# Optimization experiments

Hardware: AMD Instinct MI355X
Metric: run time of the kernel (lower is better)

## Reference

```python
import jax, jax.numpy as jnp
import numpy as np

B, S, D, H, DC, HC, M = 2, 2048, 1024, 16, 64, 16, 4096
DH = D // H  # head_dim = 64


def _ln(x, g, b, eps=1e-5):
    m = jnp.mean(x, axis=-1, keepdims=True)
    v = jnp.var(x, axis=-1, keepdims=True)
    return (x - m) * jax.lax.rsqrt(v + eps) * g + b


def setup_inputs() -> dict:
    key = jax.random.key(0)
    ks = jax.random.split(key, 10)
    def w(k, shape, fan_in):
        return jax.random.normal(k, shape, jnp.float32) * (fan_in ** -0.5)
    return {
        "h": jax.random.normal(ks[0], (B, S, D), jnp.float32),
        "z": jax.random.normal(ks[1], (B, S, DC), jnp.float32),
        # Linear weights stored [in, out] (transpose of torch layout)
        "wv": w(ks[2], (D, D), D),   "bv": jnp.zeros((D,), jnp.float32),
        "wca": w(ks[3], (DC, H * HC), DC), "bca": jnp.zeros((H * HC,), jnp.float32),
        "wcn": w(ks[4], (D, DC), D), "bcn": jnp.zeros((DC,), jnp.float32),
        "wo": w(ks[5], (D, D), D),   "bo": jnp.zeros((D,), jnp.float32),
        "gamma": jnp.zeros((1, H, 1, 1), jnp.float32),
        "w1": w(ks[6], (D, M), D),   "b1": jnp.zeros((M,), jnp.float32),
        "w2": w(ks[7], (M, D), M),   "b2": jnp.zeros((D,), jnp.float32),
        "ln1_g": jnp.ones((D,), jnp.float32),  "ln1_b": jnp.zeros((D,), jnp.float32),
        "ln2_g": jnp.ones((D,), jnp.float32),  "ln2_b": jnp.zeros((D,), jnp.float32),
        "lnc_g": jnp.ones((DC,), jnp.float32), "lnc_b": jnp.zeros((DC,), jnp.float32),
    }


def reference(h, z, wv, bv, wca, bca, wcn, bcn, wo, bo, gamma,
              w1, b1, w2, b2, ln1_g, ln1_b, ln2_g, ln2_b, lnc_g, lnc_b):
    hn = _ln(h, ln1_g, ln1_b)
    # values: [B,S,H,DH]
    value = (hn @ wv + bv).reshape(B, S, H, DH)
    # per-head coordinates: [B,S,H,HC]
    zh = (z @ wca + bca).reshape(B, S, H, HC)
    # pairwise squared distances per head: ||zq||^2 + ||zk||^2 - 2 zq.zk
    z_sq = jnp.sum(zh * zh, axis=-1).transpose(0, 2, 1)        # [B,H,S]
    dot = jnp.einsum('bqhc,bkhc->bhqk', zh, zh)                # [B,H,S,S]
    sq_dist = jnp.maximum(z_sq[:, :, :, None] + z_sq[:, :, None, :] - 2.0 * dot, 0.0)
    g = jax.nn.softplus(gamma)                                 # [1,H,1,1]
    attn = jax.nn.softmax(-g * sq_dist, axis=-1)               # [B,H,S,S]
    attn_out = jnp.einsum('bhqk,bkhd->bqhd', attn, value).reshape(B, S, D)
    h_attn = attn_out @ wo + bo
    z_next = hn @ wcn + bcn
    h = h + h_attn
    # FFN (dropout is identity in eval); torch GELU default is exact (erf)
    hn2 = _ln(h, ln2_g, ln2_b)
    ffn = jax.nn.gelu(hn2 @ w1 + b1, approximate=False) @ w2 + b2
    h = h + ffn
    z_out = _ln(z + z_next, lnc_g, lnc_b)
    return h, z_out
```

## Files before the change

### kernel.cpp

```cpp
#include <hip/hip_runtime.h>

#define USH unsigned short

__device__ __forceinline__ float b2f(USH u) {
    union { unsigned int i; float f; } x; x.i = ((unsigned int)u) << 16; return x.f;
}
__device__ __forceinline__ USH f2b(float f) {
    union { float f; unsigned int i; } x; x.f = f;
    unsigned int r = x.i + (0x7fffu + ((x.i >> 16) & 1u));
    return (USH)(r >> 16);
}
__device__ __forceinline__ float ldf(const USH* p)  { return b2f(*p); }
__device__ __forceinline__ float ldf(const float* p){ return *p; }
__device__ __forceinline__ void stf(USH* p, float v)  { *p = f2b(v); }
__device__ __forceinline__ void stf(float* p, float v){ *p = v; }

#define GLOAD16(gp, lp) __builtin_amdgcn_global_load_lds(                     \
    (const __attribute__((address_space(1))) void*)(gp),                      \
    (__attribute__((address_space(3))) void*)(lp), 16, 0, 0)

typedef __attribute__((ext_vector_type(8))) __bf16 bf16x8;
typedef __attribute__((ext_vector_type(4))) float  floatx4;

__global__ __launch_bounds__(256) void transpose_f2b(const float* __restrict__ W,
                                                     USH* __restrict__ WT,
                                                     int K, int N) {
    __shared__ USH t[64][72];
    int n0 = blockIdx.x * 64, k0 = blockIdx.y * 64;
    int tid = threadIdx.x;
    int kr = tid >> 4, nc = (tid & 15) * 4;
#pragma unroll
    for (int r = 0; r < 4; r++) {
        int k = kr + r * 16;
        float4 v = *(const float4*)(W + (size_t)(k0 + k) * N + n0 + nc);
        t[nc + 0][k] = f2b(v.x); t[nc + 1][k] = f2b(v.y);
        t[nc + 2][k] = f2b(v.z); t[nc + 3][k] = f2b(v.w);
    }
    __syncthreads();
    int nr = tid >> 2, kc = (tid & 3) * 8;
#pragma unroll
    for (int r = 0; r < 2; r++) {
        int k = kc + r * 32;
        *(int4*)(WT + (size_t)(n0 + nr) * K + k0 + k) = *(const int4*)&t[nr][k];
    }
}

template <typename TX>
__global__ __launch_bounds__(256) void ln_rows(const TX* __restrict__ x,
                                               const float* __restrict__ g,
                                               const float* __restrict__ bb,
                                               USH* __restrict__ y) {
    int row = blockIdx.x, tid = threadIdx.x;
    const TX* xr = x + (size_t)row * 1024 + tid * 4;
    float v[4];
#pragma unroll
    for (int i = 0; i < 4; i++) v[i] = ldf(xr + i);
    float s  = v[0] + v[1] + v[2] + v[3];
    float ss = v[0]*v[0] + v[1]*v[1] + v[2]*v[2] + v[3]*v[3];
#pragma unroll
    for (int o = 32; o; o >>= 1) { s += __shfl_down(s, o); ss += __shfl_down(ss, o); }
    __shared__ float red[10];
    int w = tid >> 6;
    if ((tid & 63) == 0) { red[w] = s; red[4 + w] = ss; }
    __syncthreads();
    if (tid == 0) {
        float S = red[0] + red[1] + red[2] + red[3];
        float SS = red[4] + red[5] + red[6] + red[7];
        float mean = S * (1.f / 1024.f);
        float var  = SS * (1.f / 1024.f) - mean * mean;
        red[8] = mean; red[9] = rsqrtf(var + 1e-5f);
    }
    __syncthreads();
    float mean = red[8], rstd = red[9];
    USH* yr = y + (size_t)row * 1024 + tid * 4;
#pragma unroll
    for (int i = 0; i < 4; i++) {
        int c = tid * 4 + i;
        yr[i] = f2b((v[i] - mean) * rstd * g[c] + bb[c]);
    }
}

__global__ __launch_bounds__(256) void zh_kernel(const float* __restrict__ z,
                                                 const float* __restrict__ wca,
                                                 const float* __restrict__ bca,
                                                 const float* __restrict__ gamma,
                                                 USH* __restrict__ zq_pack,
                                                 USH* __restrict__ zk_pack) {
    int row = blockIdx.x, n = threadIdx.x;
    __shared__ float zrow[64];
    if (n < 64) zrow[n] = z[(size_t)row * 64 + n];
    __syncthreads();
    float s = bca[n];
#pragma unroll 8
    for (int k = 0; k < 64; k++) s = fmaf(zrow[k], wca[(size_t)k * 256 + n], s);
    int h = n >> 4, c = n & 15;
    float gvl = log1pf(__expf(gamma[h])) * 1.44269504f;
    USH u = f2b(s);
    float sv = b2f(u);
    float sq = sv * sv;
    sq += __shfl_xor(sq, 1); sq += __shfl_xor(sq, 2);
    sq += __shfl_xor(sq, 4); sq += __shfl_xor(sq, 8);
    size_t base = ((size_t)h * 4096 + row) * 32;
    zk_pack[base + c] = u;
    zq_pack[base + c] = f2b(2.f * gvl * s);
    if (c == 0) {
        USH hi = f2b(sq);
        float lo = sq - b2f(hi);
        unsigned int kw0 = 0x3F80u | ((unsigned int)hi << 16);
        unsigned int kw1 = (unsigned int)f2b(lo);
        uint4 kv = {kw0, kw1, 0u, 0u};
        uint4 zz = {0u, 0u, 0u, 0u};
        *(uint4*)(zk_pack + base + 16) = kv;
        *(uint4*)(zk_pack + base + 24) = zz;
        unsigned int qw0 = (unsigned int)f2b(-gvl * sq) | ((unsigned int)f2b(-gvl) << 16);
        unsigned int qw1 = (unsigned int)f2b(-gvl);
        uint4 qv = {qw0, qw1, 0u, 0u};
        *(uint4*)(zq_pack + base + 16) = qv;
        *(uint4*)(zq_pack + base + 24) = zz;
    }
}

template <int EPI, int MI, int NI, int KB, typename TRES, typename TOUT>
__global__ __launch_bounds__(256) void gemm_kernel(const USH* __restrict__ A,
                                                   const USH* __restrict__ WT,
                                                   const float* __restrict__ bias,
                                                   const TRES* __restrict__ res,
                                                   TOUT* __restrict__ out,
                                                   int M, int N, int K) {
    constexpr int BM  = MI * 32;
    constexpr int BN  = NI * 32;
    constexpr int GR  = KB / 8;
    constexpr int RPC = 2048 / KB;
    constexpr int ACH = BM / RPC;
    constexpr int BCH = BN / RPC;
    __shared__ __align__(16) USH lA[BM][KB];
    __shared__ __align__(16) USH lB[BN][KB];
    int tid = threadIdx.x;
    int lane = tid & 63, wave = tid >> 6;
    int wr = wave >> 1, wc = wave & 1;
    int quad = lane >> 4, l15 = lane & 15;
    int m0 = blockIdx.x * BM, n0 = blockIdx.y * BN;

    int srow = tid / GR;
    int kg   = tid % GR;
    int scol = (kg ^ (srow & 7)) * 8;

    const USH* gA = A + (size_t)(m0 + srow) * K + scol;
    const USH* gB = WT + (size_t)(n0 + srow) * K + scol;
    USH* lA0 = &lA[0][0] + tid * 8;
    USH* lB0 = &lB[0][0] + tid * 8;
    int xo = (l15 & 7) * 8;

    floatx4 acc[MI][NI] = {};

    for (int k0 = 0; k0 < K; k0 += KB) {
#pragma unroll
        for (int c = 0; c < ACH; c++)
            GLOAD16(gA + (size_t)c * RPC * K + k0, lA0 + c * 2048);
#pragma unroll
        for (int c = 0; c < BCH; c++)
            GLOAD16(gB + (size_t)c * RPC * K + k0, lB0 + c * 2048);
        __syncthreads();

#pragma unroll
        for (int ks = 0; ks < KB / 32; ks++) {
            bf16x8 bfr[NI];
#pragma unroll
            for (int ni = 0; ni < NI; ni++)
                bfr[ni] = *(const bf16x8*)&lB[wc * (NI * 16) + ni * 16 + l15][(ks * 32 + quad * 8) ^ xo];
#pragma unroll
            for (int mi = 0; mi < MI; mi++) {
                bf16x8 afr = *(const bf16x8*)&lA[wr * (MI * 16) + mi * 16 + l15][(ks * 32 + quad * 8) ^ xo];
#pragma unroll
                for (int ni = 0; ni < NI; ni++)
                    acc[mi][ni] = __builtin_amdgcn_mfma_f32_16x16x32_bf16(afr, bfr[ni], acc[mi][ni], 0, 0, 0);
            }
        }
        __syncthreads();
    }

    float bias_v[NI];
#pragma unroll
    for (int ni = 0; ni < NI; ni++) bias_v[ni] = bias[n0 + wc * (NI * 16) + ni * 16 + l15];

#pragma unroll
    for (int mi = 0; mi < MI; mi++) {
#pragma unroll
        for (int r = 0; r < 4; r++) {
            int row = m0 + wr * (MI * 16) + mi * 16 + quad * 4 + r;
            size_t base = (size_t)row * N;
#pragma unroll
            for (int ni = 0; ni < NI; ni++) {
                int col = n0 + wc * (NI * 16) + ni * 16 + l15;
                float v = acc[mi][ni][r] + bias_v[ni];
                if (EPI == 2) {
                    float t = v * v;
                    float a = fmaf(t, -0.0713548162726f, -1.59576912161f);
                    v = v * __builtin_amdgcn_rcpf(1.f + __expf(v * a));
                }
                if (EPI == 1 || EPI == 3) v += ldf(res + base + col);
                stf(out + base + col, v);
            }
        }
    }
}

__global__ __launch_bounds__(512) void attn9_kernel(const USH* __restrict__ zq_pack,
                                                    const USH* __restrict__ zk_pack,
                                                    const USH* __restrict__ value,
                                                    USH* __restrict__ attn_out) {
    int b = blockIdx.x >> 4, h = blockIdx.x & 15;
    int q0 = blockIdx.y * 128;
    int tid = threadIdx.x, lane = tid & 63, wq = tid >> 6;
    int quad = lane >> 4, l15 = lane & 15;

    __shared__ __align__(16) USH Qb[128][40];
    __shared__ __align__(16) USH VbT[64][72];
    __shared__ __align__(16) USH Pb[8][16][72];

    const size_t zrow0 = (size_t)b * 2048;
    const USH* zq = zq_pack + ((size_t)h * 4096 + zrow0) * 32;
    const USH* zk = zk_pack + ((size_t)h * 4096 + zrow0) * 32;
    const size_t vbase = zrow0 * 1024 + h * 64;

    {
        int row = tid >> 2, c0 = (tid & 3) * 8;
        *(uint4*)&Qb[row][c0] = *(const uint4*)(zq + (size_t)(q0 + row) * 32 + c0);
    }
    __syncthreads();

    bf16x8 afragQ = *(const bf16x8*)&Qb[wq * 16 + l15][quad * 8];

    union { unsigned int u[4]; bf16x8 v; } onesu;
#pragma unroll
    for (int i = 0; i < 4; i++) onesu.u[i] = 0x3F803F80u;
    bf16x8 ones = onesu.v;

    floatx4 oacc[4] = {};
    floatx4 lacc = {};

    int key2 = (tid & 31) * 2;
    int dh0  = (tid >> 5) * 4;
    int2 vta, vtb;

    bf16x8 bk0[4], bk1[4];
#define LOADBK(dst, ktv) do {                                                  \
        int kk_ = (ktv) < 2048 ? (ktv) : 0;                                    \
        _Pragma("unroll")                                                      \
        for (int ni_ = 0; ni_ < 4; ni_++)                                      \
            dst[ni_] = *(const bf16x8*)(zk + (size_t)(kk_ + ni_ * 16 + l15) * 32 + quad * 8); \
    } while (0)

    {
        const USH* s0 = value + vbase + (size_t)key2 * 1024 + dh0;
        vta = *(const int2*)s0;
        vtb = *(const int2*)(s0 + 1024);
    }
    LOADBK(bk0, 0);

    auto body = [&](int kt, bf16x8 (&bkc)[4], bf16x8 (&bkn)[4]) {
        __syncthreads();
        {
            const USH* ua = (const USH*)&vta;
            const USH* ub = (const USH*)&vtb;
#pragma unroll
            for (int e = 0; e < 4; e++) {
                unsigned int dw = (unsigned int)ua[e] | ((unsigned int)ub[e] << 16);
                *(unsigned int*)&VbT[dh0 + e][key2] = dw;
            }
            if (kt + 64 < 2048) {
                const USH* s0 = value + vbase + (size_t)(kt + 64 + key2) * 1024 + dh0;
                vta = *(const int2*)s0;
                vtb = *(const int2*)(s0 + 1024);
            }
        }
        __syncthreads();

        floatx4 sacc[4];
#pragma unroll
        for (int ni = 0; ni < 4; ni++) {
            floatx4 zz = {};
            sacc[ni] = __builtin_amdgcn_mfma_f32_16x16x32_bf16(afragQ, bkc[ni], zz, 0, 0, 0);
        }
        LOADBK(bkn, kt + 64);

#pragma unroll
        for (int r = 0; r < 4; r++) {
#pragma unroll
            for (int ni = 0; ni < 4; ni++) {
                float pf = exp2f(sacc[ni][r]);
                union { float f; unsigned int i; } cv; cv.f = pf;
                Pb[wq][quad * 4 + r][ni * 16 + l15] = (USH)(cv.i >> 16);
            }
        }

#pragma unroll
        for (int ks2 = 0; ks2 < 2; ks2++) {
            bf16x8 bv[4];
#pragma unroll
            for (int nd = 0; nd < 4; nd++)
                bv[nd] = *(const bf16x8*)&VbT[nd * 16 + l15][ks2 * 32 + quad * 8];
            bf16x8 ap = *(const bf16x8*)&Pb[wq][l15][ks2 * 32 + quad * 8];
#pragma unroll
            for (int nd = 0; nd < 4; nd++)
                oacc[nd] = __builtin_amdgcn_mfma_f32_16x16x32_bf16(ap, bv[nd], oacc[nd], 0, 0, 0);
            lacc = __builtin_amdgcn_mfma_f32_16x16x32_bf16(ap, ones, lacc, 0, 0, 0);
        }
    };

    for (int kt = 0; kt < 2048; kt += 128) {
        body(kt, bk0, bk1);
        body(kt + 64, bk1, bk0);
    }
#undef LOADBK

#pragma unroll
    for (int r = 0; r < 4; r++) {
        float inv = 1.f / lacc[r];
        int row = q0 + wq * 16 + quad * 4 + r;
        USH* o = attn_out + (zrow0 + row) * 1024 + h * 64;
#pragma unroll
        for (int nd = 0; nd < 4; nd++) o[nd * 16 + l15] = f2b(oacc[nd][r] * inv);
    }
}

__global__ __launch_bounds__(64) void lnc_kernel(const float* __restrict__ z,
                                                 const float* __restrict__ zn,
                                                 const float* __restrict__ g,
                                                 const float* __restrict__ bb,
                                                 float* __restrict__ out) {
    int row = blockIdx.x, t = threadIdx.x;
    float v = z[(size_t)row * 64 + t] + zn[(size_t)row * 64 + t];
    float s = v, ss = v * v;
#pragma unroll
    for (int o = 32; o; o >>= 1) { s += __shfl_xor(s, o); ss += __shfl_xor(ss, o); }
    float mean = s * (1.f / 64.f);
    float rstd = rsqrtf(ss * (1.f / 64.f) - mean * mean + 1e-5f);
    out[(size_t)row * 64 + t] = (v - mean) * rstd * g[t] + bb[t];
}

extern "C" void kernel_launch(void* const* d_in, const int* in_sizes, int n_in,
                              void* d_out, int out_size, void* d_ws, size_t ws_size,
                              hipStream_t stream) {
    char* p = (char*)d_ws;
    USH*   value   = (USH*)(p);
    USH*   attn_o  = (USH*)(p + ((size_t)8  << 20));
    USH*   wcnT    = (USH*)(p + ((size_t)8  << 20));
    USH*   zq_pack = (USH*)(p + ((size_t)16 << 20));
    USH*   zk_pack = (USH*)(p + ((size_t)20 << 20));
    USH*   hn      = (USH*)(p + ((size_t)24 << 20));
    USH*   mid     = (USH*)(p);
    USH*   hn2     = (USH*)(p + ((size_t)32 << 20));
    float* znext   = (float*)(p + ((size_t)40 << 20));
    USH*   wvT     = (USH*)(p + ((size_t)41 << 20));
    USH*   woT     = (USH*)(p + ((size_t)43 << 20));
    USH*   w1T     = (USH*)(p + ((size_t)45 << 20));
    USH*   w2T     = (USH*)(p + ((size_t)53 << 20));

    const float *h    = (const float*)d_in[0],  *z    = (const float*)d_in[1];
    const float *wv   = (const float*)d_in[2],  *bv   = (const float*)d_in[3];
    const float *wca  = (const float*)d_in[4],  *bca  = (const float*)d_in[5];
    const float *wcn  = (const float*)d_in[6],  *bcn  = (const float*)d_in[7];
    const float *wo   = (const float*)d_in[8],  *bo   = (const float*)d_in[9];
    const float *gam  = (const float*)d_in[10];
    const float *w1   = (const float*)d_in[11], *b1   = (const float*)d_in[12];
    const float *w2   = (const float*)d_in[13], *b2   = (const float*)d_in[14];
    const float *ln1g = (const float*)d_in[15], *ln1b = (const float*)d_in[16];
    const float *ln2g = (const float*)d_in[17], *ln2b = (const float*)d_in[18];
    const float *lncg = (const float*)d_in[19], *lncb = (const float*)d_in[20];

    float* out_h = (float*)d_out;
    float* out_z = out_h + (size_t)4096 * 1024;
    float* h1    = out_h;

    transpose_f2b<<<dim3(16, 16), 256, 0, stream>>>(wv, wvT, 1024, 1024);
    transpose_f2b<<<dim3(16, 16), 256, 0, stream>>>(wo, woT, 1024, 1024);
    transpose_f2b<<<dim3(64, 16), 256, 0, stream>>>(w1, w1T, 1024, 4096);
    transpose_f2b<<<dim3(16, 64), 256, 0, stream>>>(w2, w2T, 4096, 1024);
    transpose_f2b<<<dim3(1, 16),  256, 0, stream>>>(wcn, wcnT, 1024, 64);

    ln_rows<float><<<4096, 256, 0, stream>>>(h, ln1g, ln1b, hn);
    zh_kernel<<<4096, 256, 0, stream>>>(z, wca, bca, gam, zq_pack, zk_pack);
    gemm_kernel<0, 4, 2, 128, USH, USH><<<dim3(32, 16), 256, 0, stream>>>(hn, wvT, bv, (const USH*)nullptr, value, 4096, 1024, 1024);
    gemm_kernel<0, 1, 1, 64, float, float><<<dim3(128, 2), 256, 0, stream>>>(hn, wcnT, bcn, (const float*)nullptr, znext, 4096, 64, 1024);
    attn9_kernel<<<dim3(32, 16), 512, 0, stream>>>(zq_pack, zk_pack, value, attn_o);
    gemm_kernel<1, 4, 2, 128, float, float><<<dim3(32, 16), 256, 0, stream>>>(attn_o, woT, bo, h, h1, 4096, 1024, 1024);
    ln_rows<float><<<4096, 256, 0, stream>>>(h1, ln2g, ln2b, hn2);
    gemm_kernel<2, 4, 4, 64, USH, USH><<<dim3(32, 32), 256, 0, stream>>>(hn2, w1T, b1, (const USH*)nullptr, mid, 4096, 4096, 1024);
    gemm_kernel<3, 4, 2, 128, float, float><<<dim3(32, 16), 256, 0, stream>>>(mid, w2T, b2, h1, out_h, 4096, 1024, 4096);
    lnc_kernel<<<4096, 64, 0, stream>>>(z, znext, lncg, lncb, out_z);
}
```

Before: 366.2 us.

## Double-buffer K and V tiles in LDS with warp-specialized loaders in attention

```diff
diff --git a/kernel.cpp b/kernel.cpp
--- a/kernel.cpp
+++ b/kernel.cpp
@@ -205,17 +205,18 @@
     }
 }
 
-__global__ __launch_bounds__(512) void attn9_kernel(const USH* __restrict__ zq_pack,
-                                                    const USH* __restrict__ zk_pack,
-                                                    const USH* __restrict__ value,
-                                                    USH* __restrict__ attn_out) {
+__global__ __launch_bounds__(512) void attn11_kernel(const USH* __restrict__ zq_pack,
+                                                     const USH* __restrict__ zk_pack,
+                                                     const USH* __restrict__ value,
+                                                     USH* __restrict__ attn_out) {
     int b = blockIdx.x >> 4, h = blockIdx.x & 15;
     int q0 = blockIdx.y * 128;
     int tid = threadIdx.x, lane = tid & 63, wq = tid >> 6;
     int quad = lane >> 4, l15 = lane & 15;
 
     __shared__ __align__(16) USH Qb[128][40];
-    __shared__ __align__(16) USH VbT[64][72];
+    __shared__ __align__(16) USH KbT[2][64][40];
+    __shared__ __align__(16) USH VbT[2][64][72];
     __shared__ __align__(16) USH Pb[8][16][72];
 
     const size_t zrow0 = (size_t)b * 2048;
@@ -239,59 +240,79 @@
     floatx4 oacc[4] = {};
     floatx4 lacc = {};
 
-    int key2 = (tid & 31) * 2;
-    int dh0  = (tid >> 5) * 4;
-    int2 vta, vtb;
-
-    bf16x8 bk0[4], bk1[4];
-#define LOADBK(dst, ktv) do {                                                  \
-        int kk_ = (ktv) < 2048 ? (ktv) : 0;                                    \
-        _Pragma("unroll")                                                      \
-        for (int ni_ = 0; ni_ < 4; ni_++)                                      \
-            dst[ni_] = *(const bf16x8*)(zk + (size_t)(kk_ + ni_ * 16 + l15) * 32 + quad * 8); \
-    } while (0)
-
-    {
-        const USH* s0 = value + vbase + (size_t)key2 * 1024 + dh0;
-        vta = *(const int2*)s0;
-        vtb = *(const int2*)(s0 + 1024);
-    }
-    LOADBK(bk0, 0);
-
-    auto body = [&](int kt, bf16x8 (&bkc)[4], bf16x8 (&bkn)[4]) {
+    int kp  = tid & 31;
+    int va  = kp & 15, vb = kp >> 4;
+    int vrow = va + vb * 32;
+    int dh0  = (tid >> 5) * 8;
+    int cb   = va * 4 + vb * 2;
+    int krow = (tid - 256) >> 2, kc0 = ((tid - 256) & 3) * 8;
+    int4 vta, vtb; uint4 kreg;
+
+    if (tid < 256) {
+        const USH* s0 = value + vbase + (size_t)vrow * 1024 + dh0;
+        vta = *(const int4*)s0;
+        vtb = *(const int4*)(s0 + 16 * 1024);
+        const USH* ua = (const USH*)&vta;
+        const USH* ub = (const USH*)&vtb;
+#pragma unroll
+        for (int e = 0; e < 8; e++) {
+            unsigned int dw = (unsigned int)ua[e] | ((unsigned int)ub[e] << 16);
+            *(unsigned int*)&VbT[0][dh0 + e][cb] = dw;
+        }
+        const USH* s1 = value + vbase + (size_t)(64 + vrow) * 1024 + dh0;
+        vta = *(const int4*)s1;
+        vtb = *(const int4*)(s1 + 16 * 1024);
+    } else {
+        kreg = *(const uint4*)(zk + (size_t)krow * 32 + kc0);
+        *(uint4*)&KbT[0][krow][kc0] = kreg;
+        kreg = *(const uint4*)(zk + (size_t)(64 + krow) * 32 + kc0);
+    }
+
+    for (int it = 0; it < 32; it++) {
+        int cur = it & 1;
         __syncthreads();
-        {
-            const USH* ua = (const USH*)&vta;
-            const USH* ub = (const USH*)&vtb;
-#pragma unroll
-            for (int e = 0; e < 4; e++) {
-                unsigned int dw = (unsigned int)ua[e] | ((unsigned int)ub[e] << 16);
-                *(unsigned int*)&VbT[dh0 + e][key2] = dw;
+        if (it + 1 < 32) {
+            if (tid < 256) {
+                const USH* ua = (const USH*)&vta;
+                const USH* ub = (const USH*)&vtb;
+#pragma unroll
+                for (int e = 0; e < 8; e++) {
+                    unsigned int dw = (unsigned int)ua[e] | ((unsigned int)ub[e] << 16);
+                    *(unsigned int*)&VbT[cur ^ 1][dh0 + e][cb] = dw;
+                }
+                if (it + 2 < 32) {
+                    const USH* s0 = value + vbase + (size_t)((it + 2) * 64 + vrow) * 1024 + dh0;
+                    vta = *(const int4*)s0;
+                    vtb = *(const int4*)(s0 + 16 * 1024);
+                }
+            } else {
+                *(uint4*)&KbT[cur ^ 1][krow][kc0] = kreg;
+                if (it + 2 < 32)
+                    kreg = *(const uint4*)(zk + (size_t)((it + 2) * 64 + krow) * 32 + kc0);
             }
-            if (kt + 64 < 2048) {
-                const USH* s0 = value + vbase + (size_t)(kt + 64 + key2) * 1024 + dh0;
-                vta = *(const int2*)s0;
-                vtb = *(const int2*)(s0 + 1024);
-            }
-        }
-        __syncthreads();
+        }
+
+        bf16x8 bk[4];
+#pragma unroll
+        for (int ni = 0; ni < 4; ni++)
+            bk[ni] = *(const bf16x8*)&KbT[cur][ni * 16 + l15][quad * 8];
 
         floatx4 sacc[4];
 #pragma unroll
         for (int ni = 0; ni < 4; ni++) {
             floatx4 zz = {};
-            sacc[ni] = __builtin_amdgcn_mfma_f32_16x16x32_bf16(afragQ, bkc[ni], zz, 0, 0, 0);
-        }
-        LOADBK(bkn, kt + 64);
+            sacc[ni] = __builtin_amdgcn_mfma_f32_16x16x32_bf16(afragQ, bk[ni], zz, 0, 0, 0);
+        }
 
 #pragma unroll
         for (int r = 0; r < 4; r++) {
-#pragma unroll
-            for (int ni = 0; ni < 4; ni++) {
-                float pf = exp2f(sacc[ni][r]);
-                union { float f; unsigned int i; } cv; cv.f = pf;
-                Pb[wq][quad * 4 + r][ni * 16 + l15] = (USH)(cv.i >> 16);
-            }
+            union { float f; unsigned int i; } c0, c1, c2, c3;
+            c0.f = exp2f(sacc[0][r]); c1.f = exp2f(sacc[1][r]);
+            c2.f = exp2f(sacc[2][r]); c3.f = exp2f(sacc[3][r]);
+            uint2 dw;
+            dw.x = (c0.i >> 16) | (c1.i & 0xFFFF0000u);
+            dw.y = (c2.i >> 16) | (c3.i & 0xFFFF0000u);
+            *(uint2*)&Pb[wq][quad * 4 + r][l15 * 4] = dw;
         }
 
 #pragma unroll
@@ -299,20 +320,14 @@
             bf16x8 bv[4];
 #pragma unroll
             for (int nd = 0; nd < 4; nd++)
-                bv[nd] = *(const bf16x8*)&VbT[nd * 16 + l15][ks2 * 32 + quad * 8];
+                bv[nd] = *(const bf16x8*)&VbT[cur][nd * 16 + l15][ks2 * 32 + quad * 8];
             bf16x8 ap = *(const bf16x8*)&Pb[wq][l15][ks2 * 32 + quad * 8];
 #pragma unroll
             for (int nd = 0; nd < 4; nd++)
                 oacc[nd] = __builtin_amdgcn_mfma_f32_16x16x32_bf16(ap, bv[nd], oacc[nd], 0, 0, 0);
             lacc = __builtin_amdgcn_mfma_f32_16x16x32_bf16(ap, ones, lacc, 0, 0, 0);
         }
-    };
-
-    for (int kt = 0; kt < 2048; kt += 128) {
-        body(kt, bk0, bk1);
-        body(kt + 64, bk1, bk0);
-    }
-#undef LOADBK
+    }
 
 #pragma unroll
     for (int r = 0; r < 4; r++) {
@@ -383,7 +398,7 @@
     zh_kernel<<<4096, 256, 0, stream>>>(z, wca, bca, gam, zq_pack, zk_pack);
     gemm_kernel<0, 4, 2, 128, USH, USH><<<dim3(32, 16), 256, 0, stream>>>(hn, wvT, bv, (const USH*)nullptr, value, 4096, 1024, 1024);
     gemm_kernel<0, 1, 1, 64, float, float><<<dim3(128, 2), 256, 0, stream>>>(hn, wcnT, bcn, (const float*)nullptr, znext, 4096, 64, 1024);
-    attn9_kernel<<<dim3(32, 16), 512, 0, stream>>>(zq_pack, zk_pack, value, attn_o);
+    attn11_kernel<<<dim3(32, 16), 512, 0, stream>>>(zq_pack, zk_pack, value, attn_o);
     gemm_kernel<1, 4, 2, 128, float, float><<<dim3(32, 16), 256, 0, stream>>>(attn_o, woT, bo, h, h1, 4096, 1024, 1024);
     ln_rows<float><<<4096, 256, 0, stream>>>(h1, ln2g, ln2b, hn2);
     gemm_kernel<2, 4, 4, 64, USH, USH><<<dim3(32, 32), 256, 0, stream>>>(hn2, w1T, b1, (const USH*)nullptr, mid, 4096, 4096, 1024);
```

After: 353.9 us. 3.4% less time.
